# Kernel optimization log

Measured on AMD Instinct MI355X. Metric: run time of the kernel, lower is better.

## Reference

```python
import jax, jax.numpy as jnp
import numpy as np

NUM_RAYS = 262144  # 512x512 image
NUM_SAMPLES = 64


def setup_inputs() -> dict:
    key = jax.random.key(0)
    k1, k2 = jax.random.split(key)
    rays_o = jax.random.normal(k1, (NUM_RAYS, 3), dtype=jnp.float32) * 0.1
    d = jax.random.normal(k2, (NUM_RAYS, 3), dtype=jnp.float32)
    rays_d = d / jnp.linalg.norm(d, axis=-1, keepdims=True)
    radii = jnp.full((1,), 1.3, dtype=jnp.float32)  # scene_radii buffer
    return {"rays_o": rays_o, "rays_d": rays_d, "radii": radii, "num_samples": NUM_SAMPLES}


def _raymarch_dense(rays_o, rays_d, radii, num_samples):
    # Ray-AABB (cube of half-extent radius) intersection + depth linspace.
    radius = radii[0]
    inv_d = 1.0 / jnp.where(rays_d == 0, jnp.full_like(rays_d, 1e-6), rays_d)
    off_neg = (-radius - rays_o) * inv_d
    off_pos = (radius - rays_o) * inv_d
    near = jnp.max(jnp.minimum(off_neg, off_pos), axis=-1, keepdims=True)  # [N,1]
    far = jnp.min(jnp.maximum(off_neg, off_pos), axis=-1, keepdims=True)   # [N,1]
    t = jnp.linspace(0.0, 1.0, num_samples, dtype=rays_o.dtype)[None]       # [1,S]
    depth = near + (far - near) * t                                         # [N,S]
    # perturb=False path (deterministic)
    samples = (rays_o[:, None, :] + rays_d[:, None, :] * depth[..., None]) / radius  # [N,S,3]
    deltas = jnp.diff(depth, axis=-1, prepend=near)                          # [N,S]
    # Concrete query_mask: occupied = inside unit sphere of normalized grid.
    mask = jnp.linalg.norm(samples, axis=-1) <= 1.0                          # [N,S] bool
    return samples, depth, deltas, mask


def reference(rays_o, rays_d, radii, num_samples):
    n = rays_o.shape[0]
    samples, depth, deltas, mask = _raymarch_dense(rays_o, rays_d, radii, num_samples)
    M = n * num_samples
    mf = mask.reshape(M)
    # Stable compaction: valid entries first, original order preserved (jnp.argsort is stable).
    order = jnp.argsort(jnp.logical_not(mf))
    num_valid = jnp.sum(mf).astype(jnp.int32)
    ridx_full = jnp.repeat(jnp.arange(n, dtype=jnp.int32), num_samples)
    ridx = ridx_full[order]                                  # [M]
    samples_c = samples.reshape(M, 3)[order]                 # [M,3]
    depth_c = depth.reshape(M)[order]                        # [M]
    deltas_c = deltas.reshape(M)[order][:, None]             # [M,1]
    valid = jnp.arange(M) < num_valid                        # padding indicator
    # mark_pack_boundaries: start of each per-ray pack
    boundary = jnp.concatenate([jnp.ones((1,), bool), ridx[1:] != ridx[:-1]]) & valid
    return ridx, samples_c, depth_c, deltas_c, boundary, num_valid
```

## Files before the change

kernel.cpp:

```cpp
#include <hip/hip_runtime.h>

#pragma clang fp contract(off)

namespace {

constexpr int S = 64;
constexpr float DELTA = 1.0f / 63.0f;

constexpr int RPB = 16;
constexpr int Q = RPB * S;
constexpr int LDSF = 7 * Q;
constexpr int LDSP = LDSF + (LDSF >> 5);

__device__ __forceinline__ int sw(int i) { return i + (i >> 5); }

__device__ __forceinline__ void ray_nearfar(
    float ox, float oy, float oz,
    float dx, float dy, float dz,
    float R, float& nr, float& fr) {
  float ix = 1.0f / ((dx == 0.0f) ? 1e-6f : dx);
  float iy = 1.0f / ((dy == 0.0f) ? 1e-6f : dy);
  float iz = 1.0f / ((dz == 0.0f) ? 1e-6f : dz);
  float mR = -R;
  float ax = (mR - ox) * ix, bx = (R - ox) * ix;
  float ay = (mR - oy) * iy, by = (R - oy) * iy;
  float az = (mR - oz) * iz, bz = (R - oz) * iz;
  nr = fmaxf(fmaxf(fminf(ax, bx), fminf(ay, by)), fminf(az, bz));
  fr = fminf(fminf(fmaxf(ax, bx), fmaxf(ay, by)), fmaxf(az, bz));
}

__global__ __launch_bounds__(256) void k_count(
    const float* __restrict__ ro, const float* __restrict__ rd,
    const float* __restrict__ radii,
    float4* __restrict__ rayinfo,
    int* __restrict__ L, int* __restrict__ blockSums, int N) {
  int r = blockIdx.x * 256 + threadIdx.x;
  int cnt = 0;
  if (r < N) {
    float R = radii[0];
    float ox = ro[3 * r], oy = ro[3 * r + 1], oz = ro[3 * r + 2];
    float dx = rd[3 * r], dy = rd[3 * r + 1], dz = rd[3 * r + 2];
    float nr, fr;
    ray_nearfar(ox, oy, oz, dx, dy, dz, R, nr, fr);
    float f = fr - nr;
    unsigned lo = 0, hi = 0;
    for (int s = 0; s < S; ++s) {
      float dep = nr + f * ((float)s * DELTA);
      float sx = (ox + dx * dep) / R;
      float sy = (oy + dy * dep) / R;
      float sz = (oz + dz * dep) / R;
      float nm = sqrtf((sx * sx + sy * sy) + sz * sz);
      unsigned bit = (nm <= 1.0f) ? 1u : 0u;
      if (s < 32) lo |= bit << s; else hi |= bit << (s - 32);
      cnt += (int)bit;
    }
    rayinfo[r] = make_float4(nr, f, __uint_as_float(lo), __uint_as_float(hi));
  }
  __shared__ int sm[256];
  sm[threadIdx.x] = cnt;
  __syncthreads();
  for (int off = 1; off < 256; off <<= 1) {
    int t = (threadIdx.x >= off) ? sm[threadIdx.x - off] : 0;
    __syncthreads();
    sm[threadIdx.x] += t;
    __syncthreads();
  }
  if (r < N) L[r] = sm[threadIdx.x] - cnt;
  if (threadIdx.x == 255) blockSums[blockIdx.x] = sm[255];
}

__global__ __launch_bounds__(1024) void k_scan(
    const int* __restrict__ blockSums, int* __restrict__ blockOff,
    int* __restrict__ total, float* __restrict__ out_nv, int nb) {
  __shared__ int sm[1024];
  int x = (threadIdx.x < nb) ? blockSums[threadIdx.x] : 0;
  sm[threadIdx.x] = x;
  __syncthreads();
  for (int off = 1; off < 1024; off <<= 1) {
    int t = (threadIdx.x >= off) ? sm[threadIdx.x - off] : 0;
    __syncthreads();
    sm[threadIdx.x] += t;
    __syncthreads();
  }
  if (threadIdx.x < nb) blockOff[threadIdx.x] = sm[threadIdx.x] - x;
  if (threadIdx.x == 1023) {
    *total = sm[1023];
    out_nv[0] = (float)sm[1023];
  }
}

__global__ __launch_bounds__(256) void k_stage(
    const float* __restrict__ ro, const float* __restrict__ rd,
    const float* __restrict__ radii,
    const float4* __restrict__ rayinfo,
    const int* __restrict__ L, const int* __restrict__ blockOff,
    const int* __restrict__ total,
    float* __restrict__ out, int N) {
  __shared__ float buf[LDSP];
  int nwg = gridDim.x;
  int chunk = nwg >> 3;
  int hw = blockIdx.x;
  int bid = (hw & 7) * chunk + (hw >> 3);
  int r0 = bid * RPB;
  int tid = threadIdx.x;
  int nv = *total;
  int V0 = L[r0] + blockOff[r0 >> 8];
  int rB = r0 + RPB;
  int VB = (rB >= N) ? nv : (L[rB] + blockOff[rB >> 8]);
  int cV = VB - V0;
  int TV = r0 * S - V0;

  int rloc = tid >> 4;
  int r = r0 + rloc;
  int s0 = (tid & 15) * 4;
  float R = radii[0];
  float4 info = rayinfo[r];
  float nr = info.x, f = info.y;
  unsigned long long msk =
      ((unsigned long long)__float_as_uint(info.w) << 32) |
      (unsigned long long)__float_as_uint(info.z);
  float ox = ro[3 * r], oy = ro[3 * r + 1], oz = ro[3 * r + 2];
  float dx = rd[3 * r], dy = rd[3 * r + 1], dz = rd[3 * r + 2];
  int Vr = L[r] + blockOff[r >> 8];
  #pragma unroll
  for (int j = 0; j < 4; ++j) {
    int s = s0 + j;
    bool bit = (msk >> s) & 1ull;
    int below = __popcll(msk & ((1ull << s) - 1ull));
    float dep = nr + f * ((float)s * DELTA);
    float sx = (ox + dx * dep) / R;
    float sy = (oy + dy * dep) / R;
    float sz = (oz + dz * dep) / R;
    float prev = (s == 0) ? nr : (nr + f * ((float)(s - 1) * DELTA));
    float del = dep - prev;
    int l = bit ? (Vr - V0 + below)
                : (cV + (r * S - Vr) - TV + (s - below));
    buf[sw(l)] = (float)r;
    buf[sw(Q + 3 * l)] = sx;
    buf[sw(Q + 3 * l + 1)] = sy;
    buf[sw(Q + 3 * l + 2)] = sz;
    buf[sw(4 * Q + l)] = dep;
    buf[sw(5 * Q + l)] = del;
    buf[sw(6 * Q + l)] = (bit && below == 0) ? 1.0f : 0.0f;
  }
  __syncthreads();

  size_t M = (size_t)N * S;
  auto wr = [&](int lds0, size_t g0, int cnt) {
    int a0 = (int)((4 - (g0 & 3)) & 3);
    if (a0 > cnt) a0 = cnt;
    int na = (cnt - a0) & ~3;
    int a1 = a0 + na;
    for (int e = tid; e < a0; e += 256) out[g0 + e] = buf[sw(lds0 + e)];
    for (int e = a1 + tid; e < cnt; e += 256) out[g0 + e] = buf[sw(lds0 + e)];
    int n4 = na >> 2;
    for (int c = tid; c < n4; c += 256) {
      int l = lds0 + a0 + 4 * c;
      float4 v = make_float4(buf[sw(l)], buf[sw(l + 1)],
                             buf[sw(l + 2)], buf[sw(l + 3)]);
      *reinterpret_cast<float4*>(out + (g0 + (size_t)a0 + 4 * (size_t)c)) = v;
    }
  };
  size_t tail0 = (size_t)nv + (size_t)TV;
  int cT = Q - cV;
  wr(0, (size_t)V0, cV);
  wr(cV, tail0, cT);
  wr(Q, M + 3 * (size_t)V0, 3 * cV);
  wr(Q + 3 * cV, M + 3 * tail0, 3 * cT);
  wr(4 * Q, 4 * M + (size_t)V0, cV);
  wr(4 * Q + cV, 4 * M + tail0, cT);
  wr(5 * Q, 5 * M + (size_t)V0, cV);
  wr(5 * Q + cV, 5 * M + tail0, cT);
  wr(6 * Q, 6 * M + (size_t)V0, cV);
  wr(6 * Q + cV, 6 * M + tail0, cT);
}

}

extern "C" void kernel_launch(void* const* d_in, const int* in_sizes, int n_in,
                              void* d_out, int out_size, void* d_ws, size_t ws_size,
                              hipStream_t stream) {
  const float* ro = (const float*)d_in[0];
  const float* rd = (const float*)d_in[1];
  const float* radii = (const float*)d_in[2];
  int N = in_sizes[0] / 3;
  int M = N * S;
  int nbA = (N + 255) / 256;

  float4* rayinfo = (float4*)d_ws;
  int* wsI = (int*)(rayinfo + N);
  int* L = wsI;
  int* blockSums = wsI + N;
  int* blockOff = blockSums + nbA;
  int* total = blockOff + nbA;

  float* out = (float*)d_out;
  float* out_nv = out + (size_t)7 * (size_t)M;

  k_count<<<nbA, 256, 0, stream>>>(ro, rd, radii, rayinfo, L, blockSums, N);
  k_scan<<<1, 1024, 0, stream>>>(blockSums, blockOff, total, out_nv, nbA);
  k_stage<<<N / RPB, 256, 0, stream>>>(ro, rd, radii, rayinfo, L, blockOff,
                                       total, out, N);
}
```

Measured before the change: 156.2 us.

## Align LDS staging segments to global alignment for vectorized float4 reads

Replaces the padded, swizzled LDS staging layout with per-array segments whose start offsets are shifted so that LDS addresses share the same 4-element alignment as their global destinations. This lets the write-out read whole float4s from LDS instead of four scalar loads, and handles the head and tail fringes with single guarded stores. The sample-to-thread mapping also changes to a strided pattern (s = lane + 16*j) to alter bank access during the scatter into LDS. Dropping the swizzle may reintroduce bank conflicts on the scattered scalar writes.

Measured after the change: 140.4 us. -10.1%, faster.

```diff
diff --git a/kernel.cpp b/kernel.cpp
--- a/kernel.cpp
+++ b/kernel.cpp
@@ -9,10 +9,7 @@
 
 constexpr int RPB = 16;
 constexpr int Q = RPB * S;
-constexpr int LDSF = 7 * Q;
-constexpr int LDSP = LDSF + (LDSF >> 5);
-
-__device__ __forceinline__ int sw(int i) { return i + (i >> 5); }
+constexpr int LDSF = 7 * Q + 5 * 16;
 
 __device__ __forceinline__ void ray_nearfar(
     float ox, float oy, float oz,
@@ -96,7 +93,7 @@
     const int* __restrict__ L, const int* __restrict__ blockOff,
     const int* __restrict__ total,
     float* __restrict__ out, int N) {
-  __shared__ float buf[LDSP];
+  __shared__ __align__(16) float buf[LDSF];
   int nwg = gridDim.x;
   int chunk = nwg >> 3;
   int hw = blockIdx.x;
@@ -108,11 +105,27 @@
   int rB = r0 + RPB;
   int VB = (rB >= N) ? nv : (L[rB] + blockOff[rB >> 8]);
   int cV = VB - V0;
+  int cT = Q - cV;
   int TV = r0 * S - V0;
+  size_t tail0 = (size_t)nv + (size_t)TV;
+  int tmod = (int)(tail0 & 3);
+
+  int Sv[5], St[5];
+  {
+    int base = 0;
+    #pragma unroll
+    for (int a = 0; a < 5; ++a) {
+      int k = (a == 1) ? 3 : 1;
+      int vm = (k * V0) & 3;
+      int tm2 = (k == 3) ? ((3 * (int)(tail0 & 3)) & 3) : tmod;
+      Sv[a] = base + vm;
+      St[a] = ((Sv[a] + k * cV + 3) & ~3) + tm2;
+      base += k * Q + 16;
+    }
+  }
 
   int rloc = tid >> 4;
   int r = r0 + rloc;
-  int s0 = (tid & 15) * 4;
   float R = radii[0];
   float4 info = rayinfo[r];
   float nr = info.x, f = info.y;
@@ -122,9 +135,10 @@
   float ox = ro[3 * r], oy = ro[3 * r + 1], oz = ro[3 * r + 2];
   float dx = rd[3 * r], dy = rd[3 * r + 1], dz = rd[3 * r + 2];
   int Vr = L[r] + blockOff[r >> 8];
+  float fr = (float)r;
   #pragma unroll
   for (int j = 0; j < 4; ++j) {
-    int s = s0 + j;
+    int s = (tid & 15) + 16 * j;
     bool bit = (msk >> s) & 1ull;
     int below = __popcll(msk & ((1ull << s) - 1ull));
     float dep = nr + f * ((float)s * DELTA);
@@ -133,15 +147,15 @@
     float sz = (oz + dz * dep) / R;
     float prev = (s == 0) ? nr : (nr + f * ((float)(s - 1) * DELTA));
     float del = dep - prev;
-    int l = bit ? (Vr - V0 + below)
-                : (cV + (r * S - Vr) - TV + (s - below));
-    buf[sw(l)] = (float)r;
-    buf[sw(Q + 3 * l)] = sx;
-    buf[sw(Q + 3 * l + 1)] = sy;
-    buf[sw(Q + 3 * l + 2)] = sz;
-    buf[sw(4 * Q + l)] = dep;
-    buf[sw(5 * Q + l)] = del;
-    buf[sw(6 * Q + l)] = (bit && below == 0) ? 1.0f : 0.0f;
+    int idxv = Vr - V0 + below;
+    int idxt = (r * S - Vr) - TV + (s - below);
+    int i1 = bit ? idxv : idxt;
+    buf[(bit ? Sv[0] : St[0]) + i1] = fr;
+    int sb = (bit ? Sv[1] : St[1]) + 3 * i1;
+    buf[sb] = sx; buf[sb + 1] = sy; buf[sb + 2] = sz;
+    buf[(bit ? Sv[2] : St[2]) + i1] = dep;
+    buf[(bit ? Sv[3] : St[3]) + i1] = del;
+    buf[(bit ? Sv[4] : St[4]) + i1] = (bit && below == 0) ? 1.0f : 0.0f;
   }
   __syncthreads();
 
@@ -149,30 +163,29 @@
   auto wr = [&](int lds0, size_t g0, int cnt) {
     int a0 = (int)((4 - (g0 & 3)) & 3);
     if (a0 > cnt) a0 = cnt;
-    int na = (cnt - a0) & ~3;
-    int a1 = a0 + na;
-    for (int e = tid; e < a0; e += 256) out[g0 + e] = buf[sw(lds0 + e)];
-    for (int e = a1 + tid; e < cnt; e += 256) out[g0 + e] = buf[sw(lds0 + e)];
-    int n4 = na >> 2;
+    int body = cnt - a0;
+    int n4 = body >> 2, rem = body & 3;
+    if (tid < a0) out[g0 + tid] = buf[lds0 + tid];
+    int l0 = lds0 + a0;
     for (int c = tid; c < n4; c += 256) {
-      int l = lds0 + a0 + 4 * c;
-      float4 v = make_float4(buf[sw(l)], buf[sw(l + 1)],
-                             buf[sw(l + 2)], buf[sw(l + 3)]);
-      *reinterpret_cast<float4*>(out + (g0 + (size_t)a0 + 4 * (size_t)c)) = v;
+      float4 v = *reinterpret_cast<const float4*>(&buf[l0 + 4 * c]);
+      *reinterpret_cast<float4*>(out + g0 + a0 + 4 * (size_t)c) = v;
+    }
+    if (tid < rem) {
+      int e = 4 * n4 + rem - 1 - tid;
+      out[g0 + a0 + e] = buf[l0 + e];
     }
   };
-  size_t tail0 = (size_t)nv + (size_t)TV;
-  int cT = Q - cV;
-  wr(0, (size_t)V0, cV);
-  wr(cV, tail0, cT);
-  wr(Q, M + 3 * (size_t)V0, 3 * cV);
-  wr(Q + 3 * cV, M + 3 * tail0, 3 * cT);
-  wr(4 * Q, 4 * M + (size_t)V0, cV);
-  wr(4 * Q + cV, 4 * M + tail0, cT);
-  wr(5 * Q, 5 * M + (size_t)V0, cV);
-  wr(5 * Q + cV, 5 * M + tail0, cT);
-  wr(6 * Q, 6 * M + (size_t)V0, cV);
-  wr(6 * Q + cV, 6 * M + tail0, cT);
+  wr(Sv[0], (size_t)V0, cV);
+  wr(St[0], tail0, cT);
+  wr(Sv[1], M + 3 * (size_t)V0, 3 * cV);
+  wr(St[1], M + 3 * tail0, 3 * cT);
+  wr(Sv[2], 4 * M + (size_t)V0, cV);
+  wr(St[2], 4 * M + tail0, cT);
+  wr(Sv[3], 5 * M + (size_t)V0, cV);
+  wr(St[3], 5 * M + tail0, cT);
+  wr(Sv[4], 6 * M + (size_t)V0, cV);
+  wr(St[4], 6 * M + tail0, cT);
 }
 
 }
```
